# Performance work log

Hardware: AMD Instinct MI355X
Metric: run time of the kernel (lower is better)

## Reference

```python
import jax, jax.numpy as jnp
import numpy as np

N, L, D = 2, 2048, 1024
H, KV, HD = 16, 4, 64
CAP = 50.0


def _rope_cache(L, hd):
    inv_freq = 1.0 / (10000.0 ** (np.arange(0, hd, 2, dtype=np.float32) / hd))
    t = np.arange(L, dtype=np.float32)
    freqs = np.outer(t, inv_freq)                      # (L, hd/2)
    emb = np.concatenate([freqs, freqs], axis=-1)      # (L, hd)
    return jnp.asarray(np.cos(emb)), jnp.asarray(np.sin(emb))


def setup_inputs() -> dict:
    key = jax.random.key(0)
    ks = jax.random.split(key, 6)
    s = 0.02
    cos, sin = _rope_cache(L, HD)
    return {
        "x": jax.random.normal(ks[0], (N, L, D), jnp.float32),
        "Wq": jax.random.normal(ks[1], (D, H * HD), jnp.float32) * s,
        "bq": jnp.zeros((H * HD,), jnp.float32),
        "Wk": jax.random.normal(ks[2], (D, KV * HD), jnp.float32) * s,
        "bk": jnp.zeros((KV * HD,), jnp.float32),
        "Wv": jax.random.normal(ks[3], (D, KV * HD), jnp.float32) * s,
        "bv": jnp.zeros((KV * HD,), jnp.float32),
        "Wo": jax.random.normal(ks[4], (D, D), jnp.float32) * s,
        "bo": jnp.zeros((D,), jnp.float32),
        "q_gamma": jnp.ones((H, HD), jnp.float32),
        "k_gamma": jnp.ones((KV, HD), jnp.float32),
        "rope_cos": cos,
        "rope_sin": sin,
        "is_causal": 1,
    }


def _rmsnorm(t, gamma):
    # t: (N, heads, L, HD); gamma: (heads, HD)
    inv = jax.lax.rsqrt(jnp.mean(t * t, axis=-1, keepdims=True) + 1e-6)
    return t * inv * gamma[None, :, None, :]


def _apply_rope(t, cos, sin):
    # t: (N, heads, L, HD); cos/sin: (L, HD)
    hd = t.shape[-1]
    t1, t2 = t[..., : hd // 2], t[..., hd // 2:]
    rot = jnp.concatenate([-t2, t1], axis=-1)
    return t * cos[None, None] + rot * sin[None, None]


def reference(x, Wq, bq, Wk, bk, Wv, bv, Wo, bo, q_gamma, k_gamma, rope_cos, rope_sin, is_causal):
    n, l, d = x.shape
    h, hd = q_gamma.shape
    kv = k_gamma.shape[0]
    n_rep = h // kv

    q = (x @ Wq + bq).reshape(n, l, h, hd).transpose(0, 2, 1, 3)   # (n,h,l,hd)
    k = (x @ Wk + bk).reshape(n, l, kv, hd).transpose(0, 2, 1, 3)  # (n,kv,l,hd)
    v = (x @ Wv + bv).reshape(n, l, kv, hd).transpose(0, 2, 1, 3)

    q = _rmsnorm(q, q_gamma)
    k = _rmsnorm(k, k_gamma)
    q = _apply_rope(q, rope_cos, rope_sin)
    k = _apply_rope(k, rope_cos, rope_sin)

    if n_rep > 1:
        k = jnp.repeat(k, n_rep, axis=1)
        v = jnp.repeat(v, n_rep, axis=1)

    scale = hd ** -0.5
    logits = jnp.einsum("bhqd,bhkd->bhqk", q, k) * scale
    logits = CAP * jnp.tanh(logits / CAP)
    if is_causal:
        causal = jnp.tril(jnp.ones((l, l), dtype=bool))
        logits = jnp.where(causal[None, None], logits, -jnp.inf)
    weights = jax.nn.softmax(logits, axis=-1)
    y = jnp.einsum("bhqk,bhkd->bhqd", weights, v)
    y = y.transpose(0, 2, 1, 3).reshape(n, l, d)
    return y @ Wo + bo
```

## Files before the change

### kernel.cpp

```cpp
#include <hip/hip_runtime.h>
#include <hip/hip_bf16.h>

typedef __attribute__((ext_vector_type(8))) short short8;
typedef __attribute__((ext_vector_type(4))) float f32x4;
typedef __attribute__((ext_vector_type(4))) unsigned int u32x4;

using bf16 = __hip_bfloat16;

#define L_SEQ 2048
#define NB 2
#define DM 1024
#define NH 16
#define NKV 4
#define HDIM 64
#define CAPV 50.0f
#define QSCALE 0.18033688f

#if __has_builtin(__builtin_amdgcn_exp2f)
#define EXP2(x) __builtin_amdgcn_exp2f(x)
#else
#define EXP2(x) exp2f(x)
#endif

__device__ __forceinline__ unsigned short f2bs(float f) {
  bf16 h = __float2bfloat16(f);
  return __builtin_bit_cast(unsigned short, h);
}

__device__ __forceinline__ float bs2f(unsigned short u) {
  return __bfloat162float(__builtin_bit_cast(bf16, u));
}

__device__ __forceinline__ unsigned int cvt_pk_bf16(float lo, float hi) {
  unsigned int w;
  asm("v_cvt_pk_bf16_f32 %0, %1, %2" : "=v"(w) : "v"(lo), "v"(hi));
  return w;
}

__device__ __forceinline__ void gload_lds16(const void* g, void* l) {
  __builtin_amdgcn_global_load_lds(
      (const __attribute__((address_space(1))) void*)g,
      (__attribute__((address_space(3))) void*)l, 16, 0, 0);
}

__global__ void k_prep(const float* __restrict__ Wq, const float* __restrict__ Wk,
                       const float* __restrict__ Wv, const float* __restrict__ Wo,
                       const float* __restrict__ x,
                       bf16* __restrict__ wqt, bf16* __restrict__ wkt,
                       bf16* __restrict__ wvt, bf16* __restrict__ wot,
                       ushort* __restrict__ xb) {
  const int z = blockIdx.z;
  const int tx = threadIdx.x, ty = threadIdx.y;
  if (z == 4) {
    const int id = blockIdx.y * 32 + blockIdx.x;
    const int tid = ty * 32 + tx;
    const size_t base = (size_t)id * 4096 + (size_t)tid * 16;
    #pragma unroll
    for (int i = 0; i < 4; ++i) {
      float4 v = *reinterpret_cast<const float4*>(x + base + i * 4);
      ushort4 o = make_ushort4(f2bs(v.x), f2bs(v.y), f2bs(v.z), f2bs(v.w));
      *reinterpret_cast<ushort4*>(xb + base + i * 4) = o;
    }
    return;
  }
  __shared__ float tile[32][33];
  const float* W = (z == 0) ? Wq : (z == 1) ? Wk : (z == 2) ? Wv : Wo;
  bf16* Wt = (z == 0) ? wqt : (z == 1) ? wkt : (z == 2) ? wvt : wot;
  const int Ncols = (z == 1 || z == 2) ? 256 : 1024;
  const int bx = blockIdx.x * 32;
  if (bx >= Ncols) return;
  const int by = blockIdx.y * 32;
  #pragma unroll
  for (int j = 0; j < 32; j += 8)
    tile[ty + j][tx] = W[(size_t)(by + ty + j) * Ncols + bx + tx];
  __syncthreads();
  #pragma unroll
  for (int j = 0; j < 32; j += 8)
    Wt[(size_t)(bx + ty + j) * 1024 + by + tx] = __float2bfloat16(tile[tx][ty + j]);
}

template<int OUT_MODE>
__global__ __launch_bounds__(256) void k_gemm(const bf16* __restrict__ A,
                                              const bf16* __restrict__ Bt,
                                              const float* __restrict__ bq,
                                              const float* __restrict__ bk,
                                              const float* __restrict__ bv,
                                              const float* __restrict__ qg,
                                              const float* __restrict__ kg,
                                              const float* __restrict__ rcT,
                                              const float* __restrict__ rsT,
                                              void* __restrict__ out0,
                                              void* __restrict__ out1,
                                              void* __restrict__ out2,
                                              const int* __restrict__ causal_flag,
                                              int M, int Ncols, int K) {
  __shared__ __align__(16) bf16 As[2][64 * 64];
  __shared__ __align__(16) bf16 Bs[2][128 * 64];
  const int t = threadIdx.x;
  const int lane = t & 63;
  const int w = t >> 6;
  const int wr = w >> 1, wc = w & 1;
  const int m0 = blockIdx.y * 64, n0 = blockIdx.x * 128;
  const int lr = lane & 15, lg = lane >> 4;
  const int nkt = K >> 6;

  bool heavy = false;
  const bf16* pO0 = nullptr;
  const bf16* pO1 = nullptr;
  const float* pdp = nullptr;
  if (OUT_MODE == 1) {
    heavy = ((*causal_flag) != 0) && ((m0 & 1024) != 0);
    pO0 = reinterpret_cast<const bf16*>(out1);
    pO1 = pO0 + (size_t)NB * L_SEQ * DM;
    pdp = reinterpret_cast<const float*>(out2);
  }

  f32x4 acc[2][4];
  #pragma unroll
  for (int m = 0; m < 2; ++m)
    #pragma unroll
    for (int n = 0; n < 4; ++n)
      acc[m][n] = f32x4{0.f, 0.f, 0.f, 0.f};

  short8 ra[2], rb[2];
  float rinv[2];
  auto issueA = [&](int kofs) {
    #pragma unroll
    for (int p = 0; p < 2; ++p) {
      const int G = p * 256 + w * 64 + lane;
      const int row = G >> 3, gc = G & 7;
      const int scol = kofs + ((gc ^ (row & 7)) * 8);
      const int grow = m0 + row;
      const int bb = grow >> 11, l = grow & 2047;
      const size_t base = ((size_t)bb * L_SEQ + l) * DM + scol;
      ra[p] = *reinterpret_cast<const short8*>(pO0 + base);
      rb[p] = *reinterpret_cast<const short8*>(pO1 + base);
      const int hh = scol >> 6;
      const float d0 = pdp[((size_t)bb * NH + hh) * L_SEQ + l];
      const float d1 = pdp[(size_t)(NB * NH) * L_SEQ + ((size_t)bb * NH + hh) * L_SEQ + l];
      rinv[p] = __builtin_amdgcn_rcpf(d0 + d1);
    }
  };
  auto writeA = [&](int buf) {
    #pragma unroll
    for (int p = 0; p < 2; ++p) {
      const int G = p * 256 + w * 64 + lane;
      const ushort* pa = reinterpret_cast<const ushort*>(&ra[p]);
      const ushort* pb = reinterpret_cast<const ushort*>(&rb[p]);
      unsigned int wo[4];
      #pragma unroll
      for (int i = 0; i < 4; ++i) {
        const float lo = (bs2f(pa[2 * i]) + bs2f(pb[2 * i])) * rinv[p];
        const float hi = (bs2f(pa[2 * i + 1]) + bs2f(pb[2 * i + 1])) * rinv[p];
        wo[i] = cvt_pk_bf16(lo, hi);
      }
      u32x4 pk = {wo[0], wo[1], wo[2], wo[3]};
      *reinterpret_cast<short8*>(&As[buf][G * 8]) = __builtin_bit_cast(short8, pk);
    }
  };
  auto gloadA = [&](int buf, int kofs) {
    #pragma unroll
    for (int p = 0; p < 2; ++p) {
      const int Gb = p * 256 + w * 64;
      const int G = Gb + lane;
      const int row = G >> 3, gc = G & 7;
      gload_lds16(&A[(size_t)(m0 + row) * K + kofs + ((gc ^ (row & 7)) * 8)],
                  &As[buf][Gb * 8]);
    }
  };
  auto gloadB = [&](int buf, int kofs) {
    #pragma unroll
    for (int p = 0; p < 4; ++p) {
      const int Gb = p * 256 + w * 64;
      const int G = Gb + lane;
      const int row = G >> 3, gc = G & 7;
      gload_lds16(&Bt[(size_t)(n0 + row) * K + kofs + ((gc ^ (row & 7)) * 8)],
                  &Bs[buf][Gb * 8]);
    }
  };
  auto mfmaStep = [&](int buf) {
    #pragma unroll
    for (int ks = 0; ks < 2; ++ks) {
      short8 af[2], bfr[4];
      #pragma unroll
      for (int m = 0; m < 2; ++m) {
        const int row = wr * 32 + m * 16 + lr;
        af[m] = *reinterpret_cast<const short8*>(
            &As[buf][row * 64 + (((ks * 4 + lg) ^ (row & 7)) * 8)]);
      }
      #pragma unroll
      for (int n = 0; n < 4; ++n) {
        const int row = wc * 64 + n * 16 + lr;
        bfr[n] = *reinterpret_cast<const short8*>(
            &Bs[buf][row * 64 + (((ks * 4 + lg) ^ (row & 7)) * 8)]);
      }
      #pragma unroll
      for (int m = 0; m < 2; ++m)
        #pragma unroll
        for (int n = 0; n < 4; ++n)
          acc[m][n] = __builtin_amdgcn_mfma_f32_16x16x32_bf16(af[m], bfr[n], acc[m][n], 0, 0, 0);
    }
  };

  int cur = 0;
  if (OUT_MODE == 1 && heavy) {
    issueA(0);
    writeA(0);
    gloadB(0, 0);
    for (int kt = 0; kt < nkt; ++kt) {
      __syncthreads();
      if (kt + 1 < nkt) {
        issueA((kt + 1) * 64);
        gloadB(cur ^ 1, (kt + 1) * 64);
      }
      mfmaStep(cur);
      if (kt + 1 < nkt) writeA(cur ^ 1);
      cur ^= 1;
    }
  } else {
    gloadA(0, 0);
    gloadB(0, 0);
    for (int kt = 0; kt < nkt; ++kt) {
      __syncthreads();
      if (kt + 1 < nkt) {
        gloadA(cur ^ 1, (kt + 1) * 64);
        gloadB(cur ^ 1, (kt + 1) * 64);
      }
      mfmaStep(cur);
      cur ^= 1;
    }
  }

  const int colbase = n0 + wc * 64;

  if (OUT_MODE == 1) {
    #pragma unroll
    for (int m = 0; m < 2; ++m) {
      const int row = m0 + wr * 32 + m * 16 + lg * 4;
      #pragma unroll
      for (int n = 0; n < 4; ++n) {
        const int col = colbase + n * 16 + lr;
        const float bvv = bq[col];
        #pragma unroll
        for (int r = 0; r < 4; ++r)
          reinterpret_cast<float*>(out0)[(size_t)(row + r) * Ncols + col] = acc[m][n][r] + bvv;
      }
    }
  } else {
    if (colbase >= 1280) {
      #pragma unroll
      for (int m = 0; m < 2; ++m) {
        const int row = m0 + wr * 32 + m * 16 + lg * 4;
        const int bb = row >> 11, l = row & 2047;
        #pragma unroll
        for (int n = 0; n < 4; ++n) {
          const int d = colbase - 1280 + n * 16 + lr;
          const float bvv = bv[d];
          ushort4 o;
          o.x = f2bs(acc[m][n][0] + bvv);
          o.y = f2bs(acc[m][n][1] + bvv);
          o.z = f2bs(acc[m][n][2] + bvv);
          o.w = f2bs(acc[m][n][3] + bvv);
          *reinterpret_cast<ushort4*>(
              &reinterpret_cast<bf16*>(out2)[((size_t)bb * 256 + d) * L_SEQ + l]) = o;
        }
      }
    } else {
      const bool isQ = (colbase < 1024);
      const float* bias = isQ ? bq : bk;
      const float* gma = isQ ? qg : kg;
      bf16* dst0 = reinterpret_cast<bf16*>(isQ ? out0 : out1);
      const int cb = isQ ? colbase : (colbase - 1024);
      const int head = cb >> 6;
      const int heads = isQ ? NH : NKV;
      const float gsc = isQ ? QSCALE : 1.0f;
      float g[4];
      #pragma unroll
      for (int n = 0; n < 4; ++n) g[n] = gma[cb + n * 16 + lr] * gsc;
      #pragma unroll
      for (int m = 0; m < 2; ++m) {
        const int row = m0 + wr * 32 + m * 16 + lg * 4;
        float vv[4][4];
        float ss[4] = {0.f, 0.f, 0.f, 0.f};
        #pragma unroll
        for (int n = 0; n < 4; ++n) {
          const float bvv = bias[cb + n * 16 + lr];
          #pragma unroll
          for (int r = 0; r < 4; ++r) {
            vv[n][r] = acc[m][n][r] + bvv;
            ss[r] = fmaf(vv[n][r], vv[n][r], ss[r]);
          }
        }
        #pragma unroll
        for (int r = 0; r < 4; ++r) {
          float s = ss[r];
          s += __shfl_xor(s, 1, 64);
          s += __shfl_xor(s, 2, 64);
          s += __shfl_xor(s, 4, 64);
          s += __shfl_xor(s, 8, 64);
          ss[r] = rsqrtf(s * (1.0f / 64.0f) + 1e-6f);
        }
        float tv[4][4];
        #pragma unroll
        for (int n = 0; n < 4; ++n)
          #pragma unroll
          for (int r = 0; r < 4; ++r)
            tv[n][r] = vv[n][r] * ss[r] * g[n];
        #pragma unroll
        for (int r = 0; r < 4; ++r) {
          const int grow = row + r;
          const int bb = grow >> 11, l = grow & 2047;
          bf16* dst = dst0 + (((size_t)bb * heads + head) * L_SEQ + l) * HDIM;
          #pragma unroll
          for (int n = 0; n < 4; ++n) {
            const int d = n * 16 + lr;
            const float c = rcT[l * HDIM + d];
            const float s2 = rsT[l * HDIM + d];
            const float rot = (n < 2) ? -tv[n ^ 2][r] : tv[n ^ 2][r];
            dst[d] = __float2bfloat16(fmaf(tv[n][r], c, rot * s2));
          }
        }
      }
    }
  }
}

__global__ __launch_bounds__(256) void k_attn(
    const bf16* __restrict__ qb, const bf16* __restrict__ kb,
    const bf16* __restrict__ vt, bf16* __restrict__ y,
    bf16* __restrict__ pO, float* __restrict__ pd,
    const int* __restrict__ causal_flag) {
  __shared__ __align__(16) bf16 Ks[2][64 * 64];
  __shared__ __align__(16) bf16 Vs[2][64 * 64];

  const int t = threadIdx.x, lane = t & 63, w = t >> 6;
  const int lr = lane & 15, lg = lane >> 4;
  const int jx = blockIdx.x;
  const int bh = blockIdx.y;
  const int half = blockIdx.z;
  const int b = bh >> 4, h = bh & 15;
  const int kvh = h >> 2;
  const bool causal = (*causal_flag) != 0;

  const int T_a = causal ? (2 * jx + 2) : 32;
  const int T_b = causal ? (32 - 2 * jx) : 32;
  const int total = T_a + T_b;
  const int mid = (total + 1) >> 1;
  const int g0 = half ? mid : 0;
  const int g1 = half ? total : mid;

  const bf16* kbase = kb + ((size_t)b * NKV + kvh) * L_SEQ * HDIM;
  const bf16* vbase = vt + ((size_t)b * NKV + kvh) * HDIM * L_SEQ;

  for (int seg = 0; seg < 2; ++seg) {
    const int qp = seg ? (15 - jx) : jx;
    const int ts = seg ? T_b : T_a;
    const int base = seg ? T_a : 0;
    const int lo = max(0, g0 - base);
    const int hi = min(ts, g1 - base);
    if (lo >= hi) continue;

    const int q0 = qp * 128;
    const int wrow = q0 + w * 32;

    short8 qf[2][2];
    #pragma unroll
    for (int s = 0; s < 2; ++s) {
      const bf16* qrow = qb + (((size_t)bh) * L_SEQ + wrow + s * 16 + lr) * HDIM;
      qf[s][0] = *reinterpret_cast<const short8*>(qrow + lg * 8);
      qf[s][1] = *reinterpret_cast<const short8*>(qrow + 32 + lg * 8);
    }

    f32x4 o0[4], o1[4];
    #pragma unroll
    for (int n = 0; n < 4; ++n) {
      o0[n] = f32x4{0.f, 0.f, 0.f, 0.f};
      o1[n] = f32x4{0.f, 0.f, 0.f, 0.f};
    }
    float plt0 = 0.f, plt1 = 0.f;

    __syncthreads();
    {
      const int k00 = lo * 64;
      #pragma unroll
      for (int i = 0; i < 2; ++i) {
        const int Gb = i * 256 + w * 64;
        const int G = Gb + lane;
        const int row = G >> 3, gc = G & 7;
        gload_lds16(kbase + (size_t)(k00 + row) * HDIM + ((gc ^ (row & 7)) * 8), &Ks[0][Gb * 8]);
        gload_lds16(vbase + (size_t)row * L_SEQ + k00 + ((gc ^ (row & 7)) * 8), &Vs[0][Gb * 8]);
      }
    }
    int cur = 0;

    for (int kt = lo; kt < hi; ++kt) {
      __syncthreads();

      if (kt + 1 < hi) {
        const int k0n = (kt + 1) * 64;
        #pragma unroll
        for (int i = 0; i < 2; ++i) {
          const int Gb = i * 256 + w * 64;
          const int G = Gb + lane;
          const int row = G >> 3, gc = G & 7;
          gload_lds16(kbase + (size_t)(k0n + row) * HDIM + ((gc ^ (row & 7)) * 8),
                      &Ks[cur ^ 1][Gb * 8]);
          gload_lds16(vbase + (size_t)row * L_SEQ + k0n + ((gc ^ (row & 7)) * 8),
                      &Vs[cur ^ 1][Gb * 8]);
        }
      }

      f32x4 s0[4], s1[4];
      #pragma unroll
      for (int n = 0; n < 4; ++n) {
        s0[n] = f32x4{0.f, 0.f, 0.f, 0.f};
        s1[n] = f32x4{0.f, 0.f, 0.f, 0.f};
      }
      #pragma unroll
      for (int n = 0; n < 4; ++n) {
        const int krow = n * 16 + lr;
        short8 kf0 = *reinterpret_cast<const short8*>(
            &Ks[cur][krow * 64 + ((lg ^ (krow & 7)) * 8)]);
        short8 kf1 = *reinterpret_cast<const short8*>(
            &Ks[cur][krow * 64 + (((4 + lg) ^ (krow & 7)) * 8)]);
        s0[n] = __builtin_amdgcn_mfma_f32_16x16x32_bf16(kf0, qf[0][0], s0[n], 0, 0, 0);
        s0[n] = __builtin_amdgcn_mfma_f32_16x16x32_bf16(kf1, qf[0][1], s0[n], 0, 0, 0);
        s1[n] = __builtin_amdgcn_mfma_f32_16x16x32_bf16(kf0, qf[1][0], s1[n], 0, 0, 0);
        s1[n] = __builtin_amdgcn_mfma_f32_16x16x32_bf16(kf1, qf[1][1], s1[n], 0, 0, 0);
      }

      const int k0 = kt * 64;
      #pragma unroll
      for (int n = 0; n < 4; ++n) {
        #pragma unroll
        for (int r = 0; r < 4; ++r) {
          float xs = s0[n][r];
          s0[n][r] = fmaf(xs, fmaf(xs * xs, -6.40607e-5f, 1.0f), -16.0f);
          xs = s1[n][r];
          s1[n][r] = fmaf(xs, fmaf(xs * xs, -6.40607e-5f, 1.0f), -16.0f);
        }
      }
      if (causal && (k0 + 63 > wrow)) {
        #pragma unroll
        for (int n = 0; n < 4; ++n) {
          const int keyb = k0 + n * 16 + lg * 4;
          #pragma unroll
          for (int r = 0; r < 4; ++r)
            if (keyb + r > wrow + lr) s0[n][r] = -1e30f;
        }
      }
      if (causal && (k0 + 63 > wrow + 16)) {
        #pragma unroll
        for (int n = 0; n < 4; ++n) {
          const int keyb = k0 + n * 16 + lg * 4;
          #pragma unroll
          for (int r = 0; r < 4; ++r)
            if (keyb + r > wrow + 16 + lr) s1[n][r] = -1e30f;
        }
      }

      unsigned int w0[8], w1[8];
      #pragma unroll
      for (int n = 0; n < 4; ++n) {
        const float a0 = EXP2(s0[n][0]);
        const float a1 = EXP2(s0[n][1]);
        const float a2 = EXP2(s0[n][2]);
        const float a3 = EXP2(s0[n][3]);
        plt0 += (a0 + a1) + (a2 + a3);
        w0[2 * n] = cvt_pk_bf16(a0, a1);
        w0[2 * n + 1] = cvt_pk_bf16(a2, a3);
        const float c0 = EXP2(s1[n][0]);
        const float c1 = EXP2(s1[n][1]);
        const float c2 = EXP2(s1[n][2]);
        const float c3 = EXP2(s1[n][3]);
        plt1 += (c0 + c1) + (c2 + c3);
        w1[2 * n] = cvt_pk_bf16(c0, c1);
        w1[2 * n + 1] = cvt_pk_bf16(c2, c3);
      }
      short8 pf0[2], pf1[2];
      #pragma unroll
      for (int ks = 0; ks < 2; ++ks) {
        u32x4 a = {w0[4 * ks], w0[4 * ks + 1], w0[4 * ks + 2], w0[4 * ks + 3]};
        u32x4 c = {w1[4 * ks], w1[4 * ks + 1], w1[4 * ks + 2], w1[4 * ks + 3]};
        pf0[ks] = __builtin_bit_cast(short8, a);
        pf1[ks] = __builtin_bit_cast(short8, c);
      }

      const int voff = 4 * (lg & 1);
      #pragma unroll
      for (int ks = 0; ks < 2; ++ks) {
        const int gA = 4 * ks + (lg >> 1);
        #pragma unroll
        for (int n = 0; n < 4; ++n) {
          const int vd = n * 16 + lr;
          const int vb_ = vd * 64;
          const int sw = vd & 7;
          const uint2 vlo = *reinterpret_cast<const uint2*>(
              &Vs[cur][vb_ + ((gA ^ sw) * 8 + voff)]);
          const uint2 vhi = *reinterpret_cast<const uint2*>(
              &Vs[cur][vb_ + (((gA + 2) ^ sw) * 8 + voff)]);
          u32x4 vv = {vlo.x, vlo.y, vhi.x, vhi.y};
          short8 vfr = __builtin_bit_cast(short8, vv);
          o0[n] = __builtin_amdgcn_mfma_f32_16x16x32_bf16(pf0[ks], vfr, o0[n], 0, 0, 0);
          o1[n] = __builtin_amdgcn_mfma_f32_16x16x32_bf16(pf1[ks], vfr, o1[n], 0, 0, 0);
        }
      }
      cur ^= 1;
    }

    const bool full = (lo == 0) && (hi == ts);
    #pragma unroll
    for (int s = 0; s < 2; ++s) {
      float ls = s ? plt1 : plt0;
      ls += __shfl_xor(ls, 16, 64);
      ls += __shfl_xor(ls, 32, 64);
      const f32x4* oa = s ? o1 : o0;
      if (full) {
        #pragma unroll
        for (int r = 0; r < 4; ++r) {
          const float den = __shfl(ls, lg * 4 + r, 64);
          const float invl = __builtin_amdgcn_rcpf(den);
          const int qg_ = wrow + s * 16 + lg * 4 + r;
          #pragma unroll
          for (int n = 0; n < 4; ++n)
            y[((size_t)b * L_SEQ + qg_) * DM + h * HDIM + n * 16 + lr] =
                __float2bfloat16(oa[n][r] * invl);
        }
      } else {
        if (lane < 16)
          pd[((size_t)half * NB * NH + bh) * L_SEQ + wrow + s * 16 + lane] = ls;
        #pragma unroll
        for (int r = 0; r < 4; ++r) {
          const int qg_ = wrow + s * 16 + lg * 4 + r;
          #pragma unroll
          for (int n = 0; n < 4; ++n)
            pO[(((size_t)half * NB + b) * L_SEQ + qg_) * DM + h * HDIM + n * 16 + lr] =
                __float2bfloat16(oa[n][r]);
        }
      }
    }
  }
}

extern "C" void kernel_launch(void* const* d_in, const int* in_sizes, int n_in,
                              void* d_out, int out_size, void* d_ws, size_t ws_size,
                              hipStream_t stream) {
  (void)in_sizes; (void)n_in; (void)out_size; (void)ws_size;
  const float* x  = (const float*)d_in[0];
  const float* Wq = (const float*)d_in[1];
  const float* bq = (const float*)d_in[2];
  const float* Wk = (const float*)d_in[3];
  const float* bk = (const float*)d_in[4];
  const float* Wv = (const float*)d_in[5];
  const float* bv = (const float*)d_in[6];
  const float* Wo = (const float*)d_in[7];
  const float* bo = (const float*)d_in[8];
  const float* qg = (const float*)d_in[9];
  const float* kg = (const float*)d_in[10];
  const float* rc = (const float*)d_in[11];
  const float* rs = (const float*)d_in[12];
  const int* causal = (const int*)d_in[13];
  float* out = (float*)d_out;

  char* ws = (char*)d_ws;
  size_t off = 0;
  auto alloc = [&](size_t bytes) -> char* {
    char* p = ws + off;
    off += (bytes + 255) & ~(size_t)255;
    return p;
  };
  bf16* xb    = (bf16*)alloc((size_t)4096 * 1024 * 2);
  bf16* wqkvt = (bf16*)alloc((size_t)1536 * 1024 * 2);
  bf16* wot   = (bf16*)alloc((size_t)1024 * 1024 * 2);
  bf16* vt    = (bf16*)alloc((size_t)NB * NKV * HDIM * L_SEQ * 2);
  bf16* qb    = (bf16*)alloc((size_t)NB * NH * L_SEQ * HDIM * 2);
  bf16* kb    = (bf16*)alloc((size_t)NB * NKV * L_SEQ * HDIM * 2);
  bf16* y     = (bf16*)alloc((size_t)4096 * 1024 * 2);
  bf16* pO    = (bf16*)alloc((size_t)2 * NB * L_SEQ * DM * 2);
  float* pd   = (float*)alloc((size_t)2 * NB * NH * L_SEQ * 4);
  bf16* wqt   = wqkvt;
  bf16* wkt   = wqkvt + (size_t)1024 * 1024;
  bf16* wvt   = wqkvt + (size_t)1280 * 1024;

  k_prep<<<dim3(32, 32, 5), dim3(32, 8), 0, stream>>>(Wq, Wk, Wv, Wo, x,
                                                      wqt, wkt, wvt, wot, (ushort*)xb);

  k_gemm<6><<<dim3(12, 64), 256, 0, stream>>>(xb, wqkvt, bq, bk, bv, qg, kg, rc, rs,
                                              qb, kb, vt, causal, 4096, 1536, 1024);

  k_attn<<<dim3(8, NB * NH, 2), 256, 0, stream>>>(qb, kb, vt, y, pO, pd, causal);

  k_gemm<1><<<dim3(8, 64), 256, 0, stream>>>(y, wot, bo, nullptr, nullptr, nullptr, nullptr,
                                             nullptr, nullptr, out, pO, pd, causal,
                                             4096, 1024, 1024);
}
```

Measured before the change: 93.43 us.

## Triple-buffer K tiles and issue prefetch after explicit vmcnt wait in attention

Restructures the attention K/V load pipeline: K moves to a three-deep LDS ring staged two tiles ahead, V stays double-buffered staged one ahead. The block barrier now comes after an explicit s_waitcnt vmcnt, and the next loads are issued right after it, so the current tile's loads are waited on precisely and the next ones overlap compute. It also raises wave priority around the MFMA sections with s_setprio. This adds LDS use, which may reduce occupancy, and relies on hand-counted vmcnt values matching the per-thread load count, which is fragile.

```diff
diff --git a/kernel.cpp b/kernel.cpp
--- a/kernel.cpp
+++ b/kernel.cpp
@@ -330,7 +330,7 @@
     const bf16* __restrict__ vt, bf16* __restrict__ y,
     bf16* __restrict__ pO, float* __restrict__ pd,
     const int* __restrict__ causal_flag) {
-  __shared__ __align__(16) bf16 Ks[2][64 * 64];
+  __shared__ __align__(16) bf16 Ks[3][64 * 64];
   __shared__ __align__(16) bf16 Vs[2][64 * 64];
 
   const int t = threadIdx.x, lane = t & 63, w = t >> 6;
@@ -352,6 +352,29 @@
   const bf16* kbase = kb + ((size_t)b * NKV + kvh) * L_SEQ * HDIM;
   const bf16* vbase = vt + ((size_t)b * NKV + kvh) * HDIM * L_SEQ;
 
+  auto stageK = [&](int j, int buf) {
+    const int kj = j * 64;
+    #pragma unroll
+    for (int i = 0; i < 2; ++i) {
+      const int Gb = i * 256 + w * 64;
+      const int G = Gb + lane;
+      const int row = G >> 3, gc = G & 7;
+      gload_lds16(kbase + (size_t)(kj + row) * HDIM + ((gc ^ (row & 7)) * 8),
+                  &Ks[buf][Gb * 8]);
+    }
+  };
+  auto stageV = [&](int j, int buf) {
+    const int kj = j * 64;
+    #pragma unroll
+    for (int i = 0; i < 2; ++i) {
+      const int Gb = i * 256 + w * 64;
+      const int G = Gb + lane;
+      const int row = G >> 3, gc = G & 7;
+      gload_lds16(vbase + (size_t)row * L_SEQ + kj + ((gc ^ (row & 7)) * 8),
+                  &Vs[buf][Gb * 8]);
+    }
+  };
+
   for (int seg = 0; seg < 2; ++seg) {
     const int qp = seg ? (15 - jx) : jx;
     const int ts = seg ? T_b : T_a;
@@ -380,35 +403,22 @@
     float plt0 = 0.f, plt1 = 0.f;
 
     __syncthreads();
-    {
-      const int k00 = lo * 64;
-      #pragma unroll
-      for (int i = 0; i < 2; ++i) {
-        const int Gb = i * 256 + w * 64;
-        const int G = Gb + lane;
-        const int row = G >> 3, gc = G & 7;
-        gload_lds16(kbase + (size_t)(k00 + row) * HDIM + ((gc ^ (row & 7)) * 8), &Ks[0][Gb * 8]);
-        gload_lds16(vbase + (size_t)row * L_SEQ + k00 + ((gc ^ (row & 7)) * 8), &Vs[0][Gb * 8]);
-      }
-    }
-    int cur = 0;
-
+    stageV(lo, 0);
+    stageK(lo, 0);
+    if (lo + 1 < hi) stageK(lo + 1, 1);
+
+    int k3 = 0, v2 = 0;
     for (int kt = lo; kt < hi; ++kt) {
-      __syncthreads();
-
       if (kt + 1 < hi) {
-        const int k0n = (kt + 1) * 64;
-        #pragma unroll
-        for (int i = 0; i < 2; ++i) {
-          const int Gb = i * 256 + w * 64;
-          const int G = Gb + lane;
-          const int row = G >> 3, gc = G & 7;
-          gload_lds16(kbase + (size_t)(k0n + row) * HDIM + ((gc ^ (row & 7)) * 8),
-                      &Ks[cur ^ 1][Gb * 8]);
-          gload_lds16(vbase + (size_t)row * L_SEQ + k0n + ((gc ^ (row & 7)) * 8),
-                      &Vs[cur ^ 1][Gb * 8]);
-        }
-      }
+        asm volatile("s_waitcnt vmcnt(2)" ::: "memory");
+      } else {
+        asm volatile("s_waitcnt vmcnt(0)" ::: "memory");
+      }
+      __builtin_amdgcn_s_barrier();
+      __builtin_amdgcn_sched_barrier(0);
+
+      if (kt + 1 < hi) stageV(kt + 1, v2 ^ 1);
+      if (kt + 2 < hi) stageK(kt + 2, (k3 + 2) % 3);
 
       f32x4 s0[4], s1[4];
       #pragma unroll
@@ -416,18 +426,20 @@
         s0[n] = f32x4{0.f, 0.f, 0.f, 0.f};
         s1[n] = f32x4{0.f, 0.f, 0.f, 0.f};
       }
+      __builtin_amdgcn_s_setprio(1);
       #pragma unroll
       for (int n = 0; n < 4; ++n) {
         const int krow = n * 16 + lr;
         short8 kf0 = *reinterpret_cast<const short8*>(
-            &Ks[cur][krow * 64 + ((lg ^ (krow & 7)) * 8)]);
+            &Ks[k3][krow * 64 + ((lg ^ (krow & 7)) * 8)]);
         short8 kf1 = *reinterpret_cast<const short8*>(
-            &Ks[cur][krow * 64 + (((4 + lg) ^ (krow & 7)) * 8)]);
+            &Ks[k3][krow * 64 + (((4 + lg) ^ (krow & 7)) * 8)]);
         s0[n] = __builtin_amdgcn_mfma_f32_16x16x32_bf16(kf0, qf[0][0], s0[n], 0, 0, 0);
         s0[n] = __builtin_amdgcn_mfma_f32_16x16x32_bf16(kf1, qf[0][1], s0[n], 0, 0, 0);
         s1[n] = __builtin_amdgcn_mfma_f32_16x16x32_bf16(kf0, qf[1][0], s1[n], 0, 0, 0);
         s1[n] = __builtin_amdgcn_mfma_f32_16x16x32_bf16(kf1, qf[1][1], s1[n], 0, 0, 0);
       }
+      __builtin_amdgcn_s_setprio(0);
 
       const int k0 = kt * 64;
       #pragma unroll
@@ -487,6 +499,7 @@
       }
 
       const int voff = 4 * (lg & 1);
+      __builtin_amdgcn_s_setprio(1);
       #pragma unroll
       for (int ks = 0; ks < 2; ++ks) {
         const int gA = 4 * ks + (lg >> 1);
@@ -496,16 +509,18 @@
           const int vb_ = vd * 64;
           const int sw = vd & 7;
           const uint2 vlo = *reinterpret_cast<const uint2*>(
-              &Vs[cur][vb_ + ((gA ^ sw) * 8 + voff)]);
+              &Vs[v2][vb_ + ((gA ^ sw) * 8 + voff)]);
           const uint2 vhi = *reinterpret_cast<const uint2*>(
-              &Vs[cur][vb_ + (((gA + 2) ^ sw) * 8 + voff)]);
+              &Vs[v2][vb_ + (((gA + 2) ^ sw) * 8 + voff)]);
           u32x4 vv = {vlo.x, vlo.y, vhi.x, vhi.y};
           short8 vfr = __builtin_bit_cast(short8, vv);
           o0[n] = __builtin_amdgcn_mfma_f32_16x16x32_bf16(pf0[ks], vfr, o0[n], 0, 0, 0);
           o1[n] = __builtin_amdgcn_mfma_f32_16x16x32_bf16(pf1[ks], vfr, o1[n], 0, 0, 0);
         }
       }
-      cur ^= 1;
+      __builtin_amdgcn_s_setprio(0);
+      k3 = (k3 == 2) ? 0 : (k3 + 1);
+      v2 ^= 1;
     }
 
     const bool full = (lo == 0) && (hi == ts);
```

After: 93.56 us, median of 2. About the same (+0.1%).
